# Optimization experiments

Hardware: AMD Instinct MI355X
Metric: run time of the kernel (lower is better)

Reference implementation:

```python
import jax, jax.numpy as jnp
import numpy as np

N_NODES = 50000
N_EDGES = 800000
IN_DIM, HID_DIM, OUT_DIM = 128, 128, 64


def setup_inputs() -> dict:
    key = jax.random.key(0)
    ks = jax.random.split(key, 12)
    x = jax.random.normal(ks[0], (N_NODES, IN_DIM), dtype=jnp.float32)
    src = jax.random.randint(ks[1], (N_EDGES,), 0, N_NODES, dtype=jnp.int32)
    dst = jax.random.randint(ks[2], (N_EDGES,), 0, N_NODES, dtype=jnp.int32)
    def lin(k, fan_in, fan_out):
        s = 1.0 / np.sqrt(fan_in)
        kw, kb = jax.random.split(k)
        W = jax.random.uniform(kw, (fan_in, fan_out), jnp.float32, -s, s)
        b = jax.random.uniform(kb, (fan_out,), jnp.float32, -s, s)
        return W, b
    W1, b1 = lin(ks[3], IN_DIM, HID_DIM)
    W2, b2 = lin(ks[4], HID_DIM, HID_DIM)
    W3, b3 = lin(ks[5], HID_DIM, OUT_DIM)
    Wf, bf = lin(ks[6], OUT_DIM, 1)
    return {"x": x, "src": src, "dst": dst,
            "W1": W1, "b1": b1, "W2": W2, "b2": b2,
            "W3": W3, "b3": b3, "Wf": Wf, "bf": bf}


def reference(x, src, dst, W1, b1, W2, b2, W3, b3, Wf, bf):
    n = x.shape[0]
    # GCN symmetric norm with self-loops: deg = in-degree + 1 (self loop)
    ones = jnp.ones(src.shape[0], x.dtype)
    deg = jax.ops.segment_sum(ones, dst, num_segments=n) + 1.0
    dinv = jax.lax.rsqrt(deg)                       # [N]
    edge_norm = dinv[src] * dinv[dst]               # [E]
    self_norm = dinv * dinv                         # [N], self-loop weight

    def gcn(h, W, b):
        h = h @ W                                   # transform first (PyG order)
        agg = jax.ops.segment_sum(h[src] * edge_norm[:, None], dst, num_segments=n)
        agg = agg + h * self_norm[:, None]          # self-loop contribution
        return agg + b

    h = jax.nn.relu(gcn(x, W1, b1))
    h = jax.nn.relu(gcn(h, W2, b2))
    h = jax.nn.relu(gcn(h, W3, b3))
    return h @ Wf + bf                              # [N, 1] per-node scores
```

## Files before the change

### kernel.cpp

```cpp
#include <hip/hip_runtime.h>
#include <hip/hip_bf16.h>

typedef short bf16x8 __attribute__((ext_vector_type(8)));
typedef float f32x4 __attribute__((ext_vector_type(4)));
typedef _Float16 f16x2 __attribute__((ext_vector_type(2)));

static __device__ __forceinline__ unsigned short f2bf_rne(float f) {
    unsigned int u = __float_as_uint(f);
    u += 0x7fff + ((u >> 16) & 1);
    return (unsigned short)(u >> 16);
}
static __device__ __forceinline__ float bf2f(unsigned short h) {
    return __uint_as_float(((unsigned int)h) << 16);
}

static __device__ __forceinline__ void wsplit_one(const float* W, unsigned short* hi,
                                                  unsigned short* lo, int BN, int idx) {
    int k = idx / BN, n = idx % BN;
    float w = W[idx];
    unsigned short h = f2bf_rne(w);
    unsigned short l = f2bf_rne(w - bf2f(h));
    int CT = BN >> 4;
    int kc = k >> 5, quad = (k >> 3) & 3, j = k & 7;
    int ct = n >> 4, c = n & 15;
    int slot = (((kc * CT + ct) * 4 + quad) * 16 + c) * 8 + j;
    hi[slot] = h;
    lo[slot] = l;
}


__global__ __launch_bounds__(256) void k_count_wsplit(const int* __restrict__ dst, int* __restrict__ deg,
                          int* __restrict__ rank,
                          const float* __restrict__ W1, const float* __restrict__ W2, const float* __restrict__ W3,
                          unsigned short* __restrict__ W1hi, unsigned short* __restrict__ W1lo,
                          unsigned short* __restrict__ W2hi, unsigned short* __restrict__ W2lo,
                          unsigned short* __restrict__ W3hi, unsigned short* __restrict__ W3lo,
                          int E) {
    int e = blockIdx.x * blockDim.x + threadIdx.x;
    if (e < E) rank[e] = atomicAdd(&deg[dst[e]], 1);
    if (e < 128 * 128) {
        wsplit_one(W1, W1hi, W1lo, 128, e);
        wsplit_one(W2, W2hi, W2lo, 128, e);
    }
    if (e < 128 * 64) wsplit_one(W3, W3hi, W3lo, 64, e);
}

__global__ __launch_bounds__(1024) void k_chunk_sums(const int* __restrict__ deg, int* __restrict__ partial,
                                                     float* __restrict__ dinv, int N) {
    __shared__ int wsum[16];
    int t = threadIdx.x;
    int i = blockIdx.x * 1024 + t;
    int v = 0;
    if (i < N) {
        int d = deg[i];
        v = d;
        dinv[i] = rsqrtf((float)d + 1.0f);
    }
    for (int off = 32; off > 0; off >>= 1) v += __shfl_down(v, off, 64);
    if ((t & 63) == 0) wsum[t >> 6] = v;
    __syncthreads();
    if (t == 0) {
        int s = 0;
        #pragma unroll
        for (int k = 0; k < 16; ++k) s += wsum[k];
        partial[blockIdx.x] = s;
    }
}

__global__ __launch_bounds__(1024) void k_chunk_scan(const int* __restrict__ deg, const int* __restrict__ partial,
                             int* __restrict__ row_start, int N, int NB) {
    __shared__ int s[1024];
    __shared__ int prefix;
    int t = threadIdx.x;
    if (t < 64) {
        int v = (t < blockIdx.x && t < NB) ? partial[t] : 0;
        for (int off = 32; off > 0; off >>= 1) v += __shfl_down(v, off, 64);
        if (t == 0) prefix = v;
    }
    int i = blockIdx.x * 1024 + t;
    int v = (i < N) ? deg[i] : 0;
    s[t] = v;
    __syncthreads();
    for (int off = 1; off < 1024; off <<= 1) {
        int x = (t >= off) ? s[t - off] : 0;
        __syncthreads();
        s[t] += x;
        __syncthreads();
    }
    if (i <= N) row_start[i] = prefix + s[t] - v;
}

__global__ __launch_bounds__(256) void k_scatter(const int* __restrict__ src, const int* __restrict__ dst,
                          const int* __restrict__ row_start, const int* __restrict__ rank,
                          const float* __restrict__ dinv,
                          int2* __restrict__ cv, int E) {
    int e = blockIdx.x * blockDim.x + threadIdx.x;
    if (e < E) {
        int d = dst[e];
        int s = src[e];
        cv[row_start[d] + rank[e]] = make_int2(s, __float_as_int(dinv[s]));
    }
}


template<int BN>
__global__ __launch_bounds__(256, 2) void k_gemm_mfma(const float* __restrict__ A,
                        const unsigned short* __restrict__ Whi, const unsigned short* __restrict__ Wlo,
                        _Float16* __restrict__ C, int N) {
    constexpr int CT = BN / 16;
    __shared__ unsigned short AhiS[4 * 64 * 8];
    __shared__ unsigned short AloS[4 * 64 * 8];
    const int tid = threadIdx.x;
    const int wave = tid >> 6;
    const int lane = tid & 63;
    const int quad = lane >> 4;
    const int c16 = lane & 15;
    const int row0 = blockIdx.x * 64;

    f32x4 acc[CT];
    #pragma unroll
    for (int t = 0; t < CT; ++t) acc[t] = (f32x4){0.f, 0.f, 0.f, 0.f};

    for (int kc = 0; kc < 4; ++kc) {
        #pragma unroll
        for (int r = 0; r < 2; ++r) {
            int f4 = tid + r * 256;
            int arow = f4 >> 3;
            int c4 = f4 & 7;
            int grow = row0 + arow;
            float4 v = make_float4(0.f, 0.f, 0.f, 0.f);
            if (grow < N) v = *(const float4*)&A[(size_t)grow * 128 + kc * 32 + c4 * 4];
            unsigned short h0 = f2bf_rne(v.x), h1 = f2bf_rne(v.y), h2 = f2bf_rne(v.z), h3 = f2bf_rne(v.w);
            ushort4 hv = make_ushort4(h0, h1, h2, h3);
            ushort4 lv = make_ushort4(f2bf_rne(v.x - bf2f(h0)), f2bf_rne(v.y - bf2f(h1)),
                                      f2bf_rne(v.z - bf2f(h2)), f2bf_rne(v.w - bf2f(h3)));
            int q = c4 >> 1;
            int joff = (c4 & 1) * 4;
            int base = (q * 64 + arow) * 8 + joff;
            *(ushort4*)&AhiS[base] = hv;
            *(ushort4*)&AloS[base] = lv;
        }
        __syncthreads();

        int abase = (quad * 64 + wave * 16 + c16) * 8;
        bf16x8 ahi = *(const bf16x8*)&AhiS[abase];
        bf16x8 alo = *(const bf16x8*)&AloS[abase];

        #pragma unroll
        for (int ct = 0; ct < CT; ++ct) {
            size_t bslot = ((size_t)(kc * CT + ct) * 64 + lane) * 8;
            bf16x8 bhi = *(const bf16x8*)&Whi[bslot];
            bf16x8 blo = *(const bf16x8*)&Wlo[bslot];
            acc[ct] = __builtin_amdgcn_mfma_f32_16x16x32_bf16(ahi, bhi, acc[ct], 0, 0, 0);
            acc[ct] = __builtin_amdgcn_mfma_f32_16x16x32_bf16(ahi, blo, acc[ct], 0, 0, 0);
            acc[ct] = __builtin_amdgcn_mfma_f32_16x16x32_bf16(alo, bhi, acc[ct], 0, 0, 0);
        }
        __syncthreads();
    }

    #pragma unroll
    for (int ct = 0; ct < CT; ++ct) {
        #pragma unroll
        for (int r = 0; r < 4; ++r) {
            int grow = row0 + wave * 16 + quad * 4 + r;
            if (grow < N) C[(size_t)grow * BN + ct * 16 + c16] = (_Float16)acc[ct][r];
        }
    }
}


__global__ __launch_bounds__(256) void k_agg128(const _Float16* __restrict__ t, float* __restrict__ outp,
                      const int* __restrict__ row_start, const int2* __restrict__ cv,
                      const float* __restrict__ dinv, const float* __restrict__ bias,
                      int N) {
    int gid = blockIdx.x * blockDim.x + threadIdx.x;
    int node = gid >> 6;
    int lane = gid & 63;
    if (node >= N) return;
    int p = row_start[node];
    int end = row_start[node + 1];
    const f16x2* tp = (const f16x2*)t;
    float2 acc[4];
    #pragma unroll
    for (int j = 0; j < 4; ++j) acc[j] = make_float2(0.f, 0.f);

    while (p < end) {
        int idx = p + lane;
        int2 h = (idx < end) ? cv[idx] : make_int2(0, 0);
        int cnt = min(end - p, 64);
        int rounds = (cnt + 15) >> 4;
        for (int r = 0; r < rounds; ++r) {
            int base = r * 16;
            int s[16]; float w[16];
            #pragma unroll
            for (int j = 0; j < 16; ++j) {
                s[j] = __builtin_amdgcn_readlane(h.x, base + j);
                w[j] = __int_as_float(__builtin_amdgcn_readlane(h.y, base + j));
            }
            f16x2 v[16];
            #pragma unroll
            for (int j = 0; j < 16; ++j) v[j] = tp[s[j] * 64 + lane];
            #pragma unroll
            for (int j = 0; j < 16; ++j) {
                acc[j & 3].x += w[j] * (float)v[j].x;
                acc[j & 3].y += w[j] * (float)v[j].y;
            }
        }
        p += 64;
    }
    float di = dinv[node];
    f16x2 sv = tp[node * 64 + lane];
    float2 bv = ((const float2*)bias)[lane];
    float sx = (acc[0].x + acc[1].x) + (acc[2].x + acc[3].x);
    float sy = (acc[0].y + acc[1].y) + (acc[2].y + acc[3].y);
    float2 r;
    r.x = fmaxf(di * sx + di * di * (float)sv.x + bv.x, 0.f);
    r.y = fmaxf(di * sy + di * di * (float)sv.y + bv.y, 0.f);
    ((float2*)outp)[node * 64 + lane] = r;
}

__global__ __launch_bounds__(256) void k_agg64_final(const _Float16* __restrict__ t, float* __restrict__ outp,
                      const int* __restrict__ row_start, const int2* __restrict__ cv,
                      const float* __restrict__ dinv, const float* __restrict__ bias,
                      const float* __restrict__ Wf, const float* __restrict__ bf,
                      int N) {
    int gid = blockIdx.x * blockDim.x + threadIdx.x;
    int node = gid >> 6;
    int lane = gid & 63;
    if (node >= N) return;
    int p = row_start[node];
    int end = row_start[node + 1];
    float acc[4] = {0.f, 0.f, 0.f, 0.f};

    while (p < end) {
        int idx = p + lane;
        int2 h = (idx < end) ? cv[idx] : make_int2(0, 0);
        int cnt = min(end - p, 64);
        int rounds = (cnt + 15) >> 4;
        for (int r = 0; r < rounds; ++r) {
            int base = r * 16;
            int s[16]; float w[16];
            #pragma unroll
            for (int j = 0; j < 16; ++j) {
                s[j] = __builtin_amdgcn_readlane(h.x, base + j);
                w[j] = __int_as_float(__builtin_amdgcn_readlane(h.y, base + j));
            }
            _Float16 v[16];
            #pragma unroll
            for (int j = 0; j < 16; ++j) v[j] = t[s[j] * 64 + lane];
            #pragma unroll
            for (int j = 0; j < 16; ++j) acc[j & 3] += w[j] * (float)v[j];
        }
        p += 64;
    }
    float di = dinv[node];
    float r = di * ((acc[0] + acc[1]) + (acc[2] + acc[3])) + di * di * (float)t[node * 64 + lane] + bias[lane];
    r = fmaxf(r, 0.f);
    float v = r * Wf[lane];
    for (int off = 32; off > 0; off >>= 1) v += __shfl_down(v, off, 64);
    if (lane == 0) outp[node] = v + bf[0];
}


extern "C" void kernel_launch(void* const* d_in, const int* in_sizes, int n_in,
                              void* d_out, int out_size, void* d_ws, size_t ws_size,
                              hipStream_t stream) {
    const float* x  = (const float*)d_in[0];
    const int*   src = (const int*)d_in[1];
    const int*   dst = (const int*)d_in[2];
    const float* W1 = (const float*)d_in[3];
    const float* b1 = (const float*)d_in[4];
    const float* W2 = (const float*)d_in[5];
    const float* b2 = (const float*)d_in[6];
    const float* W3 = (const float*)d_in[7];
    const float* b3 = (const float*)d_in[8];
    const float* Wf = (const float*)d_in[9];
    const float* bf = (const float*)d_in[10];
    float* out = (float*)d_out;

    const int N = 50000;
    const int E = 800000;

    char* ws = (char*)d_ws;
    size_t off = 0;
    auto alloc = [&](size_t bytes) -> void* {
        void* p = (void*)(ws + off);
        off += (bytes + 511) & ~((size_t)511);
        return p;
    };
    int*   deg       = (int*)alloc((size_t)N * 4);
    float* dinv      = (float*)alloc((size_t)N * 4);
    int*   row_start = (int*)alloc((size_t)(N + 1) * 4);
    int*   partial   = (int*)alloc(64 * 4);
    int*   rank      = (int*)alloc((size_t)E * 4);
    int2*  cv        = (int2*)alloc((size_t)E * 8);
    _Float16* bufT   = (_Float16*)alloc((size_t)N * 128 * 2);
    float* bufH      = (float*)alloc((size_t)N * 128 * 4);
    unsigned short* W1hi = (unsigned short*)alloc(128 * 128 * 2);
    unsigned short* W1lo = (unsigned short*)alloc(128 * 128 * 2);
    unsigned short* W2hi = (unsigned short*)alloc(128 * 128 * 2);
    unsigned short* W2lo = (unsigned short*)alloc(128 * 128 * 2);
    unsigned short* W3hi = (unsigned short*)alloc(128 * 64 * 2);
    unsigned short* W3lo = (unsigned short*)alloc(128 * 64 * 2);

    hipMemsetAsync(deg, 0, (size_t)N * 4, stream);

    k_count_wsplit<<<(E + 255) / 256, 256, 0, stream>>>(dst, deg, rank, W1, W2, W3,
                                                        W1hi, W1lo, W2hi, W2lo, W3hi, W3lo, E);
    int NB = (N + 1023) / 1024;
    k_chunk_sums<<<NB, 1024, 0, stream>>>(deg, partial, dinv, N);
    k_chunk_scan<<<NB, 1024, 0, stream>>>(deg, partial, row_start, N, NB);
    k_scatter<<<(E + 255) / 256, 256, 0, stream>>>(src, dst, row_start, rank, dinv, cv, E);

    int gemmGrid = (N + 63) / 64;
    int aggGrid = (N * 64 + 255) / 256;

    k_gemm_mfma<128><<<gemmGrid, 256, 0, stream>>>(x, W1hi, W1lo, bufT, N);
    k_agg128<<<aggGrid, 256, 0, stream>>>(bufT, bufH, row_start, cv, dinv, b1, N);
    k_gemm_mfma<128><<<gemmGrid, 256, 0, stream>>>(bufH, W2hi, W2lo, bufT, N);
    k_agg128<<<aggGrid, 256, 0, stream>>>(bufT, bufH, row_start, cv, dinv, b2, N);
    k_gemm_mfma<64><<<gemmGrid, 256, 0, stream>>>(bufH, W3hi, W3lo, bufT, N);
    k_agg64_final<<<aggGrid, 256, 0, stream>>>(bufT, out, row_start, cv, dinv, b3, Wf, bf, N);
}
```

Baseline: 279.2 us.

## Merge degree scan kernels and double GEMM row tile per block

Two degree-scan kernels become one. Each block now recomputes its prefix by summing every preceding degree directly, so the partial-sums kernel and one launch go away, at the cost of redundant global reads in later blocks. The MFMA GEMM now handles 128 rows per block (32 per wave) instead of 64, so each weight fragment loaded from global is reused across two row tiles. This cuts weight traffic and halves the grid, but uses more registers and LDS per block.

```diff
diff --git a/kernel.cpp b/kernel.cpp
--- a/kernel.cpp
+++ b/kernel.cpp
@@ -45,40 +45,34 @@
     if (e < 128 * 64) wsplit_one(W3, W3hi, W3lo, 64, e);
 }
 
-__global__ __launch_bounds__(1024) void k_chunk_sums(const int* __restrict__ deg, int* __restrict__ partial,
-                                                     float* __restrict__ dinv, int N) {
+__global__ __launch_bounds__(1024) void k_scan(const int* __restrict__ deg, float* __restrict__ dinv,
+                                               int* __restrict__ row_start, int N) {
+    __shared__ int s[1024];
     __shared__ int wsum[16];
-    int t = threadIdx.x;
-    int i = blockIdx.x * 1024 + t;
+    __shared__ int prefix;
+    const int t = threadIdx.x;
+    const int base = blockIdx.x * 1024;
+
+    {
+        int v = 0;
+        for (int j = t; j < base; j += 1024) v += deg[j];
+        for (int off = 32; off > 0; off >>= 1) v += __shfl_down(v, off, 64);
+        if ((t & 63) == 0) wsum[t >> 6] = v;
+        __syncthreads();
+        if (t == 0) {
+            int acc = 0;
+            #pragma unroll
+            for (int k = 0; k < 16; ++k) acc += wsum[k];
+            prefix = acc;
+        }
+    }
+
+    int i = base + t;
     int v = 0;
     if (i < N) {
-        int d = deg[i];
-        v = d;
-        dinv[i] = rsqrtf((float)d + 1.0f);
-    }
-    for (int off = 32; off > 0; off >>= 1) v += __shfl_down(v, off, 64);
-    if ((t & 63) == 0) wsum[t >> 6] = v;
-    __syncthreads();
-    if (t == 0) {
-        int s = 0;
-        #pragma unroll
-        for (int k = 0; k < 16; ++k) s += wsum[k];
-        partial[blockIdx.x] = s;
-    }
-}
-
-__global__ __launch_bounds__(1024) void k_chunk_scan(const int* __restrict__ deg, const int* __restrict__ partial,
-                             int* __restrict__ row_start, int N, int NB) {
-    __shared__ int s[1024];
-    __shared__ int prefix;
-    int t = threadIdx.x;
-    if (t < 64) {
-        int v = (t < blockIdx.x && t < NB) ? partial[t] : 0;
-        for (int off = 32; off > 0; off >>= 1) v += __shfl_down(v, off, 64);
-        if (t == 0) prefix = v;
-    }
-    int i = blockIdx.x * 1024 + t;
-    int v = (i < N) ? deg[i] : 0;
+        v = deg[i];
+        dinv[i] = rsqrtf((float)v + 1.0f);
+    }
     s[t] = v;
     __syncthreads();
     for (int off = 1; off < 1024; off <<= 1) {
@@ -108,22 +102,24 @@
                         const unsigned short* __restrict__ Whi, const unsigned short* __restrict__ Wlo,
                         _Float16* __restrict__ C, int N) {
     constexpr int CT = BN / 16;
-    __shared__ unsigned short AhiS[4 * 64 * 8];
-    __shared__ unsigned short AloS[4 * 64 * 8];
+    __shared__ unsigned short AhiS[4 * 128 * 8];
+    __shared__ unsigned short AloS[4 * 128 * 8];
     const int tid = threadIdx.x;
     const int wave = tid >> 6;
     const int lane = tid & 63;
     const int quad = lane >> 4;
     const int c16 = lane & 15;
-    const int row0 = blockIdx.x * 64;
-
-    f32x4 acc[CT];
+    const int row0 = blockIdx.x * 128;
+
+    f32x4 acc[2][CT];
     #pragma unroll
-    for (int t = 0; t < CT; ++t) acc[t] = (f32x4){0.f, 0.f, 0.f, 0.f};
+    for (int m = 0; m < 2; ++m)
+        #pragma unroll
+        for (int t = 0; t < CT; ++t) acc[m][t] = (f32x4){0.f, 0.f, 0.f, 0.f};
 
     for (int kc = 0; kc < 4; ++kc) {
         #pragma unroll
-        for (int r = 0; r < 2; ++r) {
+        for (int r = 0; r < 4; ++r) {
             int f4 = tid + r * 256;
             int arow = f4 >> 3;
             int c4 = f4 & 7;
@@ -136,34 +132,44 @@
                                       f2bf_rne(v.z - bf2f(h2)), f2bf_rne(v.w - bf2f(h3)));
             int q = c4 >> 1;
             int joff = (c4 & 1) * 4;
-            int base = (q * 64 + arow) * 8 + joff;
+            int base = (q * 128 + arow) * 8 + joff;
             *(ushort4*)&AhiS[base] = hv;
             *(ushort4*)&AloS[base] = lv;
         }
         __syncthreads();
 
-        int abase = (quad * 64 + wave * 16 + c16) * 8;
-        bf16x8 ahi = *(const bf16x8*)&AhiS[abase];
-        bf16x8 alo = *(const bf16x8*)&AloS[abase];
+        int r0 = wave * 32 + c16;
+        int abase0 = (quad * 128 + r0) * 8;
+        int abase1 = (quad * 128 + r0 + 16) * 8;
+        bf16x8 ahi0 = *(const bf16x8*)&AhiS[abase0];
+        bf16x8 alo0 = *(const bf16x8*)&AloS[abase0];
+        bf16x8 ahi1 = *(const bf16x8*)&AhiS[abase1];
+        bf16x8 alo1 = *(const bf16x8*)&AloS[abase1];
 
         #pragma unroll
         for (int ct = 0; ct < CT; ++ct) {
             size_t bslot = ((size_t)(kc * CT + ct) * 64 + lane) * 8;
             bf16x8 bhi = *(const bf16x8*)&Whi[bslot];
             bf16x8 blo = *(const bf16x8*)&Wlo[bslot];
-            acc[ct] = __builtin_amdgcn_mfma_f32_16x16x32_bf16(ahi, bhi, acc[ct], 0, 0, 0);
-            acc[ct] = __builtin_amdgcn_mfma_f32_16x16x32_bf16(ahi, blo, acc[ct], 0, 0, 0);
-            acc[ct] = __builtin_amdgcn_mfma_f32_16x16x32_bf16(alo, bhi, acc[ct], 0, 0, 0);
+            acc[0][ct] = __builtin_amdgcn_mfma_f32_16x16x32_bf16(ahi0, bhi, acc[0][ct], 0, 0, 0);
+            acc[0][ct] = __builtin_amdgcn_mfma_f32_16x16x32_bf16(ahi0, blo, acc[0][ct], 0, 0, 0);
+            acc[0][ct] = __builtin_amdgcn_mfma_f32_16x16x32_bf16(alo0, bhi, acc[0][ct], 0, 0, 0);
+            acc[1][ct] = __builtin_amdgcn_mfma_f32_16x16x32_bf16(ahi1, bhi, acc[1][ct], 0, 0, 0);
+            acc[1][ct] = __builtin_amdgcn_mfma_f32_16x16x32_bf16(ahi1, blo, acc[1][ct], 0, 0, 0);
+            acc[1][ct] = __builtin_amdgcn_mfma_f32_16x16x32_bf16(alo1, bhi, acc[1][ct], 0, 0, 0);
         }
         __syncthreads();
     }
 
     #pragma unroll
-    for (int ct = 0; ct < CT; ++ct) {
+    for (int m = 0; m < 2; ++m) {
         #pragma unroll
-        for (int r = 0; r < 4; ++r) {
-            int grow = row0 + wave * 16 + quad * 4 + r;
-            if (grow < N) C[(size_t)grow * BN + ct * 16 + c16] = (_Float16)acc[ct][r];
+        for (int ct = 0; ct < CT; ++ct) {
+            #pragma unroll
+            for (int r = 0; r < 4; ++r) {
+                int grow = row0 + wave * 32 + m * 16 + quad * 4 + r;
+                if (grow < N) C[(size_t)grow * BN + ct * 16 + c16] = (_Float16)acc[m][ct][r];
+            }
         }
     }
 }
@@ -291,7 +297,6 @@
     int*   deg       = (int*)alloc((size_t)N * 4);
     float* dinv      = (float*)alloc((size_t)N * 4);
     int*   row_start = (int*)alloc((size_t)(N + 1) * 4);
-    int*   partial   = (int*)alloc(64 * 4);
     int*   rank      = (int*)alloc((size_t)E * 4);
     int2*  cv        = (int2*)alloc((size_t)E * 8);
     _Float16* bufT   = (_Float16*)alloc((size_t)N * 128 * 2);
@@ -308,11 +313,10 @@
     k_count_wsplit<<<(E + 255) / 256, 256, 0, stream>>>(dst, deg, rank, W1, W2, W3,
                                                         W1hi, W1lo, W2hi, W2lo, W3hi, W3lo, E);
     int NB = (N + 1023) / 1024;
-    k_chunk_sums<<<NB, 1024, 0, stream>>>(deg, partial, dinv, N);
-    k_chunk_scan<<<NB, 1024, 0, stream>>>(deg, partial, row_start, N, NB);
+    k_scan<<<NB, 1024, 0, stream>>>(deg, dinv, row_start, N);
     k_scatter<<<(E + 255) / 256, 256, 0, stream>>>(src, dst, row_start, rank, dinv, cv, E);
 
-    int gemmGrid = (N + 63) / 64;
+    int gemmGrid = (N + 127) / 128;
     int aggGrid = (N * 64 + 255) / 256;
 
     k_gemm_mfma<128><<<gemmGrid, 256, 0, stream>>>(x, W1hi, W1lo, bufT, N);
```

Result: slower. 296.5 us (+6.2%).

## Merge scan kernels and co-launch edge scatter with first GEMM

Applied to the files above, without the earlier changes.

The two-pass degree scan is replaced by a single kernel in which each block recomputes its prefix by summing all earlier degrees directly. The edge scatter into CSR is folded into the first GEMM launch as extra blocks, so the independent scatter and GEMM work share one grid. This removes two kernel launches and lets scatter overlap with GEMM. In exchange, later scan blocks do redundant prefix reads (up to about 50K ints each), and the fused kernel carries the GEMM's launch bounds and shared memory for the scatter blocks too.

```diff
diff --git a/kernel.cpp b/kernel.cpp
--- a/kernel.cpp
+++ b/kernel.cpp
@@ -29,93 +29,18 @@
 }
 
 
-__global__ __launch_bounds__(256) void k_count_wsplit(const int* __restrict__ dst, int* __restrict__ deg,
-                          int* __restrict__ rank,
-                          const float* __restrict__ W1, const float* __restrict__ W2, const float* __restrict__ W3,
-                          unsigned short* __restrict__ W1hi, unsigned short* __restrict__ W1lo,
-                          unsigned short* __restrict__ W2hi, unsigned short* __restrict__ W2lo,
-                          unsigned short* __restrict__ W3hi, unsigned short* __restrict__ W3lo,
-                          int E) {
-    int e = blockIdx.x * blockDim.x + threadIdx.x;
-    if (e < E) rank[e] = atomicAdd(&deg[dst[e]], 1);
-    if (e < 128 * 128) {
-        wsplit_one(W1, W1hi, W1lo, 128, e);
-        wsplit_one(W2, W2hi, W2lo, 128, e);
-    }
-    if (e < 128 * 64) wsplit_one(W3, W3hi, W3lo, 64, e);
-}
-
-__global__ __launch_bounds__(1024) void k_chunk_sums(const int* __restrict__ deg, int* __restrict__ partial,
-                                                     float* __restrict__ dinv, int N) {
-    __shared__ int wsum[16];
-    int t = threadIdx.x;
-    int i = blockIdx.x * 1024 + t;
-    int v = 0;
-    if (i < N) {
-        int d = deg[i];
-        v = d;
-        dinv[i] = rsqrtf((float)d + 1.0f);
-    }
-    for (int off = 32; off > 0; off >>= 1) v += __shfl_down(v, off, 64);
-    if ((t & 63) == 0) wsum[t >> 6] = v;
-    __syncthreads();
-    if (t == 0) {
-        int s = 0;
-        #pragma unroll
-        for (int k = 0; k < 16; ++k) s += wsum[k];
-        partial[blockIdx.x] = s;
-    }
-}
-
-__global__ __launch_bounds__(1024) void k_chunk_scan(const int* __restrict__ deg, const int* __restrict__ partial,
-                             int* __restrict__ row_start, int N, int NB) {
-    __shared__ int s[1024];
-    __shared__ int prefix;
-    int t = threadIdx.x;
-    if (t < 64) {
-        int v = (t < blockIdx.x && t < NB) ? partial[t] : 0;
-        for (int off = 32; off > 0; off >>= 1) v += __shfl_down(v, off, 64);
-        if (t == 0) prefix = v;
-    }
-    int i = blockIdx.x * 1024 + t;
-    int v = (i < N) ? deg[i] : 0;
-    s[t] = v;
-    __syncthreads();
-    for (int off = 1; off < 1024; off <<= 1) {
-        int x = (t >= off) ? s[t - off] : 0;
-        __syncthreads();
-        s[t] += x;
-        __syncthreads();
-    }
-    if (i <= N) row_start[i] = prefix + s[t] - v;
-}
-
-__global__ __launch_bounds__(256) void k_scatter(const int* __restrict__ src, const int* __restrict__ dst,
-                          const int* __restrict__ row_start, const int* __restrict__ rank,
-                          const float* __restrict__ dinv,
-                          int2* __restrict__ cv, int E) {
-    int e = blockIdx.x * blockDim.x + threadIdx.x;
-    if (e < E) {
-        int d = dst[e];
-        int s = src[e];
-        cv[row_start[d] + rank[e]] = make_int2(s, __float_as_int(dinv[s]));
-    }
-}
-
-
 template<int BN>
-__global__ __launch_bounds__(256, 2) void k_gemm_mfma(const float* __restrict__ A,
+static __device__ __forceinline__ void gemm_body(const float* __restrict__ A,
                         const unsigned short* __restrict__ Whi, const unsigned short* __restrict__ Wlo,
-                        _Float16* __restrict__ C, int N) {
+                        _Float16* __restrict__ C, int N, int blk,
+                        unsigned short* AhiS, unsigned short* AloS) {
     constexpr int CT = BN / 16;
-    __shared__ unsigned short AhiS[4 * 64 * 8];
-    __shared__ unsigned short AloS[4 * 64 * 8];
     const int tid = threadIdx.x;
     const int wave = tid >> 6;
     const int lane = tid & 63;
     const int quad = lane >> 4;
     const int c16 = lane & 15;
-    const int row0 = blockIdx.x * 64;
+    const int row0 = blk * 64;
 
     f32x4 acc[CT];
     #pragma unroll
@@ -169,6 +94,92 @@
 }
 
 
+__global__ __launch_bounds__(256) void k_count_wsplit(const int* __restrict__ dst, int* __restrict__ deg,
+                          int* __restrict__ rank,
+                          const float* __restrict__ W1, const float* __restrict__ W2, const float* __restrict__ W3,
+                          unsigned short* __restrict__ W1hi, unsigned short* __restrict__ W1lo,
+                          unsigned short* __restrict__ W2hi, unsigned short* __restrict__ W2lo,
+                          unsigned short* __restrict__ W3hi, unsigned short* __restrict__ W3lo,
+                          int E) {
+    int e = blockIdx.x * blockDim.x + threadIdx.x;
+    if (e < E) rank[e] = atomicAdd(&deg[dst[e]], 1);
+    if (e < 128 * 128) {
+        wsplit_one(W1, W1hi, W1lo, 128, e);
+        wsplit_one(W2, W2hi, W2lo, 128, e);
+    }
+    if (e < 128 * 64) wsplit_one(W3, W3hi, W3lo, 64, e);
+}
+
+__global__ __launch_bounds__(1024) void k_scan(const int* __restrict__ deg, float* __restrict__ dinv,
+                                               int* __restrict__ row_start, int N) {
+    __shared__ int s[1024];
+    __shared__ int wsum[16];
+    __shared__ int prefix;
+    const int t = threadIdx.x;
+    const int base = blockIdx.x * 1024;
+
+    {
+        int v = 0;
+        for (int j = t; j < base; j += 1024) v += deg[j];
+        for (int off = 32; off > 0; off >>= 1) v += __shfl_down(v, off, 64);
+        if ((t & 63) == 0) wsum[t >> 6] = v;
+        __syncthreads();
+        if (t == 0) {
+            int acc = 0;
+            #pragma unroll
+            for (int k = 0; k < 16; ++k) acc += wsum[k];
+            prefix = acc;
+        }
+    }
+
+    int i = base + t;
+    int v = 0;
+    if (i < N) {
+        v = deg[i];
+        dinv[i] = rsqrtf((float)v + 1.0f);
+    }
+    s[t] = v;
+    __syncthreads();
+    for (int off = 1; off < 1024; off <<= 1) {
+        int x = (t >= off) ? s[t - off] : 0;
+        __syncthreads();
+        s[t] += x;
+        __syncthreads();
+    }
+    if (i <= N) row_start[i] = prefix + s[t] - v;
+}
+
+
+__global__ __launch_bounds__(256, 2) void k_gemm1_scatter(const float* __restrict__ A,
+                          const unsigned short* __restrict__ Whi, const unsigned short* __restrict__ Wlo,
+                          _Float16* __restrict__ C, int N, int gemmGrid,
+                          const int* __restrict__ src, const int* __restrict__ dst,
+                          const int* __restrict__ row_start, const int* __restrict__ rank,
+                          const float* __restrict__ dinv, int2* __restrict__ cv, int E) {
+    __shared__ unsigned short AhiS[4 * 64 * 8];
+    __shared__ unsigned short AloS[4 * 64 * 8];
+    if ((int)blockIdx.x < gemmGrid) {
+        gemm_body<128>(A, Whi, Wlo, C, N, blockIdx.x, AhiS, AloS);
+    } else {
+        int e = (blockIdx.x - gemmGrid) * 256 + threadIdx.x;
+        if (e < E) {
+            int d = dst[e];
+            int s = src[e];
+            cv[row_start[d] + rank[e]] = make_int2(s, __float_as_int(dinv[s]));
+        }
+    }
+}
+
+template<int BN>
+__global__ __launch_bounds__(256, 2) void k_gemm_mfma(const float* __restrict__ A,
+                        const unsigned short* __restrict__ Whi, const unsigned short* __restrict__ Wlo,
+                        _Float16* __restrict__ C, int N) {
+    __shared__ unsigned short AhiS[4 * 64 * 8];
+    __shared__ unsigned short AloS[4 * 64 * 8];
+    gemm_body<BN>(A, Whi, Wlo, C, N, blockIdx.x, AhiS, AloS);
+}
+
+
 __global__ __launch_bounds__(256) void k_agg128(const _Float16* __restrict__ t, float* __restrict__ outp,
                       const int* __restrict__ row_start, const int2* __restrict__ cv,
                       const float* __restrict__ dinv, const float* __restrict__ bias,
@@ -291,7 +302,6 @@
     int*   deg       = (int*)alloc((size_t)N * 4);
     float* dinv      = (float*)alloc((size_t)N * 4);
     int*   row_start = (int*)alloc((size_t)(N + 1) * 4);
-    int*   partial   = (int*)alloc(64 * 4);
     int*   rank      = (int*)alloc((size_t)E * 4);
     int2*  cv        = (int2*)alloc((size_t)E * 8);
     _Float16* bufT   = (_Float16*)alloc((size_t)N * 128 * 2);
@@ -308,14 +318,14 @@
     k_count_wsplit<<<(E + 255) / 256, 256, 0, stream>>>(dst, deg, rank, W1, W2, W3,
                                                         W1hi, W1lo, W2hi, W2lo, W3hi, W3lo, E);
     int NB = (N + 1023) / 1024;
-    k_chunk_sums<<<NB, 1024, 0, stream>>>(deg, partial, dinv, N);
-    k_chunk_scan<<<NB, 1024, 0, stream>>>(deg, partial, row_start, N, NB);
-    k_scatter<<<(E + 255) / 256, 256, 0, stream>>>(src, dst, row_start, rank, dinv, cv, E);
+    k_scan<<<NB, 1024, 0, stream>>>(deg, dinv, row_start, N);
 
     int gemmGrid = (N + 63) / 64;
+    int scatGrid = (E + 255) / 256;
     int aggGrid = (N * 64 + 255) / 256;
 
-    k_gemm_mfma<128><<<gemmGrid, 256, 0, stream>>>(x, W1hi, W1lo, bufT, N);
+    k_gemm1_scatter<<<gemmGrid + scatGrid, 256, 0, stream>>>(x, W1hi, W1lo, bufT, N, gemmGrid,
+                                                             src, dst, row_start, rank, dinv, cv, E);
     k_agg128<<<aggGrid, 256, 0, stream>>>(bufT, bufH, row_start, cv, dinv, b1, N);
     k_gemm_mfma<128><<<gemmGrid, 256, 0, stream>>>(bufH, W2hi, W2lo, bufT, N);
     k_agg128<<<aggGrid, 256, 0, stream>>>(bufT, bufH, row_start, cv, dinv, b2, N);
```

Result: no change. 276.3 us (-1.0%).
